# Kernel optimization log

Hardware: AMD Instinct MI355X
Metric: run time of the kernel (lower is better)

Reference implementation:

```python
import jax, jax.numpy as jnp
import numpy as np

N_NODES = 100000
N_EDGES = 3200000
EPS = 1e-5


def gcn_conv(x, edge_index, W, b):
    # PyG GCNConv: sym-normalized A+I, transform-then-propagate
    h = x @ W                                   # [N, out]
    src, dst = edge_index[0], edge_index[1]
    ones = jnp.ones(edge_index.shape[1], dtype=x.dtype)
    deg = jax.ops.segment_sum(ones, dst, num_segments=N_NODES) + 1.0  # +1 self-loop
    dis = jax.lax.rsqrt(deg)                    # deg^{-1/2}
    coef = (dis[src] * dis[dst])[:, None]
    agg = jax.ops.segment_sum(h[src] * coef, dst, num_segments=N_NODES)
    agg = agg + h * (dis * dis)[:, None]        # self-loop contribution
    return agg + b


def batch_norm(x, gamma, beta):
    mu = jnp.mean(x, axis=0)
    var = jnp.mean(jnp.square(x - mu), axis=0)
    return (x - mu) * jax.lax.rsqrt(var + EPS) * gamma + beta


def setup_inputs() -> dict:
    key = jax.random.key(0)
    ks = jax.random.split(key, 12)
    d = {
        "x": jax.random.normal(ks[0], (N_NODES, 256), dtype=jnp.float32),
        "edge_index": jax.random.randint(ks[1], (2, N_EDGES), 0, N_NODES, dtype=jnp.int32),
        "W1": jax.random.normal(ks[2], (256, 128), dtype=jnp.float32) * (1.0 / np.sqrt(256)),
        "b1": jnp.zeros((128,), jnp.float32),
        "g1": jnp.ones((128,), jnp.float32),
        "bt1": jnp.zeros((128,), jnp.float32),
        "W2": jax.random.normal(ks[3], (128, 64), dtype=jnp.float32) * (1.0 / np.sqrt(128)),
        "b2": jnp.zeros((64,), jnp.float32),
        "g2": jnp.ones((64,), jnp.float32),
        "bt2": jnp.zeros((64,), jnp.float32),
        "W3": jax.random.normal(ks[4], (64, 32), dtype=jnp.float32) * (1.0 / np.sqrt(64)),
        "b3": jnp.zeros((32,), jnp.float32),
        "g3": jnp.ones((32,), jnp.float32),
        "bt3": jnp.zeros((32,), jnp.float32),
        "Wfc": jax.random.normal(ks[5], (32, 1), dtype=jnp.float32) * (1.0 / np.sqrt(32)),
        "bfc": jnp.zeros((1,), jnp.float32),
    }
    return d


def reference(x, edge_index, W1, b1, g1, bt1, W2, b2, g2, bt2, W3, b3, g3, bt3, Wfc, bfc):
    h = jax.nn.relu(batch_norm(gcn_conv(x, edge_index, W1, b1), g1, bt1))
    h = jax.nn.relu(batch_norm(gcn_conv(h, edge_index, W2, b2), g2, bt2))
    h = jax.nn.relu(batch_norm(gcn_conv(h, edge_index, W3, b3), g3, bt3))
    return h @ Wfc + bfc
```

## Files before the change

kernel.cpp:

```cpp
#include <hip/hip_runtime.h>
#include <hip/hip_fp16.h>

#define EPS 1e-5f
constexpr int NT = 256;
constexpr int BSH = 9;
constexpr int BNODES = 1 << BSH;
constexpr int CH = 4096;

typedef _Float16 v8h __attribute__((ext_vector_type(8)));
typedef float v4f __attribute__((ext_vector_type(4)));


__global__ __launch_bounds__(NT) void bhist_kernel(const int* __restrict__ dst, int* __restrict__ gbhist,
                                                   int E, int NBUK) {
    __shared__ int h[512];
    int tid = threadIdx.x;
    for (int i = tid; i < 512; i += NT) h[i] = 0;
    __syncthreads();
    for (int e = blockIdx.x * NT + tid; e < E; e += gridDim.x * NT)
        atomicAdd(&h[dst[e] >> BSH], 1);
    __syncthreads();
    for (int i = tid; i < NBUK; i += NT)
        if (h[i]) atomicAdd(&gbhist[i], h[i]);
}


__global__ __launch_bounds__(NT) void bscan_kernel(const int* __restrict__ gbhist, int* __restrict__ bbase,
                                                   int* __restrict__ gcur, int E, int NBUK) {
    __shared__ int wsum[5];
    int tid = threadIdx.x;
    int lane = tid & 63, wid = tid >> 6;
    int e0 = (2 * tid < NBUK) ? gbhist[2 * tid] : 0;
    int e1 = (2 * tid + 1 < NBUK) ? gbhist[2 * tid + 1] : 0;
    int u = e0 + e1;
    int incl = u;
    #pragma unroll
    for (int off = 1; off < 64; off <<= 1) {
        int t = __shfl_up(incl, off, 64);
        if (lane >= off) incl += t;
    }
    if (lane == 63) wsum[wid] = incl;
    __syncthreads();
    if (tid == 0) { int s = 0; for (int w = 0; w < 4; w++) { int t = wsum[w]; wsum[w] = s; s += t; } }
    __syncthreads();
    int base = wsum[wid] + incl - u;
    if (2 * tid < NBUK)     { bbase[2 * tid] = base;          gcur[2 * tid] = base; }
    if (2 * tid + 1 < NBUK) { bbase[2 * tid + 1] = base + e0; gcur[2 * tid + 1] = base + e0; }
    if (tid == 0) bbase[NBUK] = E;
}


__global__ __launch_bounds__(NT) void part_kernel(const int* __restrict__ src, const int* __restrict__ dst,
                                                  int* __restrict__ gcur, int2* __restrict__ ebuf,
                                                  int E, int NBUK) {
    constexpr int EPT = CH / NT;
    __shared__ int hist[512];
    __shared__ int lscan[512];
    __shared__ int gbase[512];
    __shared__ int2 stage[CH];
    int tid = threadIdx.x;
    int lane = tid & 63;
    int e0 = blockIdx.x * CH;

    for (int i = tid; i < 512; i += NT) hist[i] = 0;
    __syncthreads();

    int2 ed[EPT]; int rank[EPT]; int buk[EPT];
    #pragma unroll
    for (int j = 0; j < EPT; j++) {
        int e = e0 + j * NT + tid;
        if (e < E) {
            ed[j].x = src[e]; ed[j].y = dst[e];
            buk[j] = ed[j].y >> BSH;
            rank[j] = atomicAdd(&hist[buk[j]], 1);
        } else buk[j] = -1;
    }
    __syncthreads();
    if (tid < 64) {
        int bi = tid * 8;
        int v[8]; int s = 0;
        #pragma unroll
        for (int j = 0; j < 8; j++) { v[j] = s; s += hist[bi + j]; }
        int incl = s;
        #pragma unroll
        for (int off = 1; off < 64; off <<= 1) {
            int t = __shfl_up(incl, off, 64);
            if (lane >= off) incl += t;
        }
        int lb = incl - s;
        #pragma unroll
        for (int j = 0; j < 8; j++) lscan[bi + j] = lb + v[j];
    }
    __syncthreads();
    for (int i = tid; i < NBUK; i += NT) {
        int c = hist[i];
        gbase[i] = c ? atomicAdd(&gcur[i], c) : 0;
    }
    #pragma unroll
    for (int j = 0; j < EPT; j++)
        if (buk[j] >= 0) stage[lscan[buk[j]] + rank[j]] = ed[j];
    __syncthreads();
    int cnt = min(E - e0, CH);
    for (int i = tid; i < cnt; i += NT) {
        int2 e = stage[i];
        int b = e.y >> BSH;
        ebuf[gbase[b] + (i - lscan[b])] = e;
    }
}


__global__ __launch_bounds__(NT) void bfill_kernel(const int2* __restrict__ ebuf, const int* __restrict__ bbase,
                                                   int* __restrict__ deg, int* __restrict__ row_start,
                                                   float* __restrict__ dis, int* __restrict__ csr, int N) {
    __shared__ int ldeg[BNODES];
    __shared__ int lrs[BNODES];
    __shared__ int wsum[5];
    int tid = threadIdx.x;
    int lane = tid & 63, wid = tid >> 6;
    int b = blockIdx.x;
    int node0 = b << BSH;
    int nn = min(BNODES, N - node0);
    int beg = bbase[b], end = bbase[b + 1];

    for (int i = tid; i < BNODES; i += NT) ldeg[i] = 0;
    __syncthreads();
    for (int i = beg + tid; i < end; i += NT)
        atomicAdd(&ldeg[ebuf[i].y - node0], 1);
    __syncthreads();
    int e0 = ldeg[2 * tid], e1 = ldeg[2 * tid + 1];
    int u = e0 + e1;
    int incl = u;
    #pragma unroll
    for (int off = 1; off < 64; off <<= 1) {
        int t = __shfl_up(incl, off, 64);
        if (lane >= off) incl += t;
    }
    if (lane == 63) wsum[wid] = incl;
    __syncthreads();
    if (tid == 0) { int s = 0; for (int w = 0; w < 4; w++) { int t = wsum[w]; wsum[w] = s; s += t; } }
    __syncthreads();
    int base = wsum[wid] + incl - u;
    lrs[2 * tid] = base;
    lrs[2 * tid + 1] = base + e0;
    __syncthreads();
    for (int i = tid; i < nn; i += NT) {
        int dg = ldeg[i];
        deg[node0 + i] = dg;
        row_start[node0 + i] = beg + lrs[i];
        dis[node0 + i] = rsqrtf((float)dg + 1.0f);
    }
    __syncthreads();
    for (int i = tid; i < BNODES; i += NT) ldeg[i] = 0;
    __syncthreads();
    for (int i = beg + tid; i < end; i += NT) {
        int2 e = ebuf[i];
        int l = e.y - node0;
        int off = atomicAdd(&ldeg[l], 1);
        csr[beg + lrs[l] + off] = e.x;
    }
}


__global__ __launch_bounds__(NT) void prepw_kernel(const float* __restrict__ W1, const float* __restrict__ W2,
                                                   const float* __restrict__ W3, __half* __restrict__ Wt1,
                                                   __half* __restrict__ Wt2, __half* __restrict__ Wt3) {
    int i = blockIdx.x * NT + threadIdx.x;
    if (i < 256 * 128) {
        int k = i >> 7, f = i & 127;
        Wt1[f * 256 + k] = __float2half(W1[i]);
    } else if (i < 256 * 128 + 128 * 64) {
        int j = i - 256 * 128; int k = j >> 6, f = j & 63;
        Wt2[f * 128 + k] = __float2half(W2[j]);
    } else if (i < 256 * 128 + 128 * 64 + 64 * 32) {
        int j = i - 256 * 128 - 128 * 64; int k = j >> 5, f = j & 31;
        Wt3[f * 64 + k] = __float2half(W3[j]);
    }
}


template<int K, int F, bool NORM>
__global__ __launch_bounds__(NT) void mgemm_kernel(const void* __restrict__ Xv, const __half* __restrict__ Wt,
                                                   const float* __restrict__ dis, const float* __restrict__ an,
                                                   const float* __restrict__ cn, __half* __restrict__ out, int N) {
    constexpr int KC = 32;
    constexpr int CG = F / 16;
    constexpr int LDA = KC + 8;
    constexpr int ASZ = NORM ? K : 1;
    __shared__ __half As[64 * LDA];
    __shared__ __half Bs[F * LDA];
    __shared__ float as_[ASZ], cs_[ASZ];

    int tid = threadIdx.x;
    if constexpr (NORM) {
        for (int i = tid; i < K; i += NT) { as_[i] = an[i]; cs_[i] = cn[i]; }
        __syncthreads();
    }
    int row0 = blockIdx.x * 64;
    int wid = tid >> 6, lane = tid & 63;
    int quad = lane >> 4, l16 = lane & 15;
    int tr = tid >> 3;
    int tk = (tid & 7) * 4;

    v4f acc[CG];
    #pragma unroll
    for (int g = 0; g < CG; g++) acc[g] = (v4f)0.f;

    for (int k0 = 0; k0 < K; k0 += KC) {
        #pragma unroll
        for (int r = tr; r < 64; r += 32) {
            int row = row0 + r;
            __half h0, h1, h2, h3;
            if (row < N) {
                if constexpr (NORM) {
                    const __half2* xp = (const __half2*)((const __half*)Xv + (size_t)row * K + k0 + tk);
                    float2 v0 = __half22float2(xp[0]);
                    float2 v1 = __half22float2(xp[1]);
                    h0 = __float2half(fmaxf(v0.x * as_[k0 + tk]     + cs_[k0 + tk],     0.f));
                    h1 = __float2half(fmaxf(v0.y * as_[k0 + tk + 1] + cs_[k0 + tk + 1], 0.f));
                    h2 = __float2half(fmaxf(v1.x * as_[k0 + tk + 2] + cs_[k0 + tk + 2], 0.f));
                    h3 = __float2half(fmaxf(v1.y * as_[k0 + tk + 3] + cs_[k0 + tk + 3], 0.f));
                } else {
                    float4 v = *(const float4*)((const float*)Xv + (size_t)row * K + k0 + tk);
                    h0 = __float2half(v.x); h1 = __float2half(v.y);
                    h2 = __float2half(v.z); h3 = __float2half(v.w);
                }
            } else {
                h0 = h1 = h2 = h3 = __float2half(0.f);
            }
            __half2* dst = (__half2*)&As[r * LDA + tk];
            dst[0] = __halves2half2(h0, h1);
            dst[1] = __halves2half2(h2, h3);
        }
        #pragma unroll
        for (int n = tr; n < F; n += 32) {
            const __half2* wp = (const __half2*)(Wt + (size_t)n * K + k0 + tk);
            __half2* dst = (__half2*)&Bs[n * LDA + tk];
            dst[0] = wp[0];
            dst[1] = wp[1];
        }
        __syncthreads();
        v8h a = *(const v8h*)&As[(wid * 16 + l16) * LDA + quad * 8];
        #pragma unroll
        for (int g = 0; g < CG; g++) {
            v8h b = *(const v8h*)&Bs[(g * 16 + l16) * LDA + quad * 8];
            acc[g] = __builtin_amdgcn_mfma_f32_16x16x32_f16(a, b, acc[g], 0, 0, 0);
        }
        __syncthreads();
    }
    #pragma unroll
    for (int reg = 0; reg < 4; reg++) {
        int row = row0 + wid * 16 + quad * 4 + reg;
        if (row < N) {
            float d = dis[row];
            #pragma unroll
            for (int g = 0; g < CG; g++)
                out[(size_t)row * F + g * 16 + l16] = __float2half(d * acc[g][reg]);
        }
    }
}


template<int F, int U>
__global__ __launch_bounds__(NT) void agg_kernel(const __half* __restrict__ hd, const int* __restrict__ csr,
                                                 const int* __restrict__ row_start, const int* __restrict__ deg,
                                                 const float* __restrict__ dis, const float* __restrict__ b,
                                                 __half* __restrict__ pre, int N) {
    constexpr int H = F / 2;
    constexpr int EPI = 64 / H;
    int wid = (blockIdx.x * NT + threadIdx.x) >> 6;
    int lane = threadIdx.x & 63;
    int fpos = lane % H;
    int sub = lane / H;
    if (wid >= N) return;
    int node = wid;
    int beg = row_start[node];
    int cnt = deg[node];
    const __half2* __restrict__ hd2 = (const __half2*)hd;

    float sx[U], sy[U];
    #pragma unroll
    for (int u = 0; u < U; u++) { sx[u] = 0.f; sy[u] = 0.f; }
    if (sub == 0) {
        float2 f = __half22float2(hd2[(size_t)node * H + fpos]);
        sx[0] = f.x; sy[0] = f.y;
    }
    int i = 0;
    for (; i + EPI * U <= cnt; i += EPI * U) {
        int srcs[U];
        #pragma unroll
        for (int u = 0; u < U; u++) srcs[u] = csr[beg + i + u * EPI + sub];
        #pragma unroll
        for (int u = 0; u < U; u++) {
            float2 f = __half22float2(hd2[(size_t)srcs[u] * H + fpos]);
            sx[u] += f.x; sy[u] += f.y;
        }
    }
    for (; i + sub < cnt; i += EPI) {
        int s = csr[beg + i + sub];
        float2 f = __half22float2(hd2[(size_t)s * H + fpos]);
        sx[0] += f.x; sy[0] += f.y;
    }
    #pragma unroll
    for (int u = 1; u < U; u++) { sx[0] += sx[u]; sy[0] += sy[u]; }
    #pragma unroll
    for (int m = H; m < 64; m <<= 1) {
        sx[0] += __shfl_xor(sx[0], m, 64);
        sy[0] += __shfl_xor(sy[0], m, 64);
    }
    if (sub == 0) {
        float d = dis[node];
        float2 bv = ((const float2*)b)[fpos];
        ((__half2*)pre)[(size_t)node * H + fpos] =
            __floats2half2_rn(d * sx[0] + bv.x, d * sy[0] + bv.y);
    }
}


template<int F>
__global__ __launch_bounds__(NT) void stats_kernel(const __half* __restrict__ pre, float* __restrict__ S1,
                                                   float* __restrict__ S2, int N) {
    constexpr int RPB = NT / F;
    int tid = threadIdx.x;
    int f = tid % F, r0 = tid / F;
    float s1 = 0.f, s2 = 0.f;
    for (int node = blockIdx.x * RPB + r0; node < N; node += gridDim.x * RPB) {
        float v = __half2float(pre[(size_t)node * F + f]);
        s1 += v; s2 += v * v;
    }
    __shared__ float l1[NT], l2[NT];
    l1[tid] = s1; l2[tid] = s2;
    __syncthreads();
    if (tid < F) {
        #pragma unroll
        for (int j = 1; j < RPB; j++) { s1 += l1[tid + j * F]; s2 += l2[tid + j * F]; }
        atomicAdd(&S1[tid], s1);
        atomicAdd(&S2[tid], s2);
    }
}

__global__ void params_kernel(const float* __restrict__ S1, const float* __restrict__ S2,
                              const float* __restrict__ g, const float* __restrict__ bt,
                              float* __restrict__ a, float* __restrict__ c, int N, int F) {
    int f = threadIdx.x;
    if (f < F) {
        float inv = 1.0f / (float)N;
        float mu = S1[f] * inv;
        float var = fmaxf(S2[f] * inv - mu * mu, 0.f);
        float av = g[f] * rsqrtf(var + EPS);
        a[f] = av;
        c[f] = bt[f] - mu * av;
    }
}


__global__ __launch_bounds__(NT) void fc_kernel(const __half* __restrict__ pre, const float* __restrict__ a,
                                                const float* __restrict__ c, const float* __restrict__ wfc,
                                                const float* __restrict__ bfc, float* __restrict__ out, int N) {
    __shared__ float wa[32], wc[32], ww[32];
    int tid = threadIdx.x;
    if (tid < 32) { wa[tid] = a[tid]; wc[tid] = c[tid]; ww[tid] = wfc[tid]; }
    __syncthreads();
    int n = blockIdx.x * NT + tid;
    if (n >= N) return;
    const __half2* p = (const __half2*)(pre + (size_t)n * 32);
    float acc = bfc[0];
    #pragma unroll
    for (int i = 0; i < 16; i++) {
        float2 v = __half22float2(p[i]);
        int f = i * 2;
        acc += fmaxf(v.x * wa[f] + wc[f], 0.f) * ww[f];
        acc += fmaxf(v.y * wa[f + 1] + wc[f + 1], 0.f) * ww[f + 1];
    }
    out[n] = acc;
}


extern "C" void kernel_launch(void* const* d_in, const int* in_sizes, int n_in,
                              void* d_out, int out_size, void* d_ws, size_t ws_size,
                              hipStream_t stream) {
    const float* x   = (const float*)d_in[0];
    const int*   ei  = (const int*)d_in[1];
    const float* W1  = (const float*)d_in[2];
    const float* b1  = (const float*)d_in[3];
    const float* g1  = (const float*)d_in[4];
    const float* bt1 = (const float*)d_in[5];
    const float* W2  = (const float*)d_in[6];
    const float* b2  = (const float*)d_in[7];
    const float* g2  = (const float*)d_in[8];
    const float* bt2 = (const float*)d_in[9];
    const float* W3  = (const float*)d_in[10];
    const float* b3  = (const float*)d_in[11];
    const float* g3  = (const float*)d_in[12];
    const float* bt3 = (const float*)d_in[13];
    const float* Wfc = (const float*)d_in[14];
    const float* bfc = (const float*)d_in[15];
    float* out = (float*)d_out;

    int N = in_sizes[0] / 256;
    int E = in_sizes[1] / 2;
    const int* src = ei;
    const int* dst = ei + E;
    int NBUK = (N + BNODES - 1) >> BSH;

    char* ws = (char*)d_ws;
    size_t off = 0;
    auto alloc = [&](size_t bytes) -> char* {
        char* p = ws + off;
        off += (bytes + 255) & ~(size_t)255;
        return p;
    };
    __half* bufA     = (__half*)alloc((size_t)N * 128 * 2);
    __half* bufB     = (__half*)alloc((size_t)N * 128 * 2);
    int2*  ebuf      = (int2*)alloc((size_t)E * 8);
    int*   csr       = (int*)alloc((size_t)E * 4);
    int*   deg       = (int*)alloc((size_t)N * 4);
    int*   row_start = (int*)alloc((size_t)N * 4);
    float* dis       = (float*)alloc((size_t)N * 4);
    int*   gbhist    = (int*)alloc((size_t)NBUK * 4);
    int*   bbase     = (int*)alloc((size_t)(NBUK + 1) * 4);
    int*   gcur      = (int*)alloc((size_t)NBUK * 4);
    __half* Wt1      = (__half*)alloc(256 * 128 * 2);
    __half* Wt2      = (__half*)alloc(128 * 64 * 2);
    __half* Wt3      = (__half*)alloc(64 * 32 * 2);
    float* stats = (float*)alloc(448 * 4 * 2);
    float* S1_1 = stats;       float* S2_1 = S1_1 + 128;
    float* S1_2 = S2_1 + 128;  float* S2_2 = S1_2 + 64;
    float* S1_3 = S2_2 + 64;   float* S2_3 = S1_3 + 32;
    float* a1 = S2_3 + 32; float* c1 = a1 + 128;
    float* a2 = c1 + 128;  float* c2 = a2 + 64;
    float* a3 = c2 + 64;   float* c3 = a3 + 32;

    hipMemsetAsync(gbhist, 0, (size_t)NBUK * 4, stream);
    hipMemsetAsync(stats, 0, 448 * 4, stream);

    bhist_kernel<<<512, NT, 0, stream>>>(dst, gbhist, E, NBUK);
    bscan_kernel<<<1, NT, 0, stream>>>(gbhist, bbase, gcur, E, NBUK);
    part_kernel<<<(E + CH - 1) / CH, NT, 0, stream>>>(src, dst, gcur, ebuf, E, NBUK);
    bfill_kernel<<<NBUK, NT, 0, stream>>>(ebuf, bbase, deg, row_start, dis, csr, N);
    prepw_kernel<<<(256 * 128 + 128 * 64 + 64 * 32 + NT - 1) / NT, NT, 0, stream>>>(W1, W2, W3, Wt1, Wt2, Wt3);

    int GB = (N + 63) / 64;
    int AB = (N + 3) / 4;
    int NB = (N + NT - 1) / NT;
    mgemm_kernel<256, 128, false><<<GB, NT, 0, stream>>>(x, Wt1, dis, nullptr, nullptr, bufA, N);
    agg_kernel<128, 4><<<AB, NT, 0, stream>>>(bufA, csr, row_start, deg, dis, b1, bufB, N);
    stats_kernel<128><<<256, NT, 0, stream>>>(bufB, S1_1, S2_1, N);
    params_kernel<<<1, 128, 0, stream>>>(S1_1, S2_1, g1, bt1, a1, c1, N, 128);
    mgemm_kernel<128, 64, true><<<GB, NT, 0, stream>>>(bufB, Wt2, dis, a1, c1, bufA, N);
    agg_kernel<64, 4><<<AB, NT, 0, stream>>>(bufA, csr, row_start, deg, dis, b2, bufB, N);
    stats_kernel<64><<<256, NT, 0, stream>>>(bufB, S1_2, S2_2, N);
    params_kernel<<<1, 64, 0, stream>>>(S1_2, S2_2, g2, bt2, a2, c2, N, 64);
    mgemm_kernel<64, 32, true><<<GB, NT, 0, stream>>>(bufB, Wt3, dis, a2, c2, bufA, N);
    agg_kernel<32, 2><<<AB, NT, 0, stream>>>(bufA, csr, row_start, deg, dis, b3, bufB, N);
    stats_kernel<32><<<256, NT, 0, stream>>>(bufB, S1_3, S2_3, N);
    params_kernel<<<1, 32, 0, stream>>>(S1_3, S2_3, g3, bt3, a3, c3, N, 32);
    fc_kernel<<<NB, NT, 0, stream>>>(bufB, a3, c3, Wfc, bfc, out, N);
}
```

Baseline: 683.5 us.

## Widen aggregation gathers to 16-byte loads and pack edge buffer into ints

The aggregation kernel now has each lane gather eight half-precision features with one 128-bit load, so one wavefront processes several edges at once. It still reduces across sub-groups with shuffles, and unroll factors are retuned per layer. The edge partition buffer packs the local destination offset and the source index into a single 32-bit word, halving its traffic, and the stats kernel reads half2 pairs. The packing assumes source indices fit in 18 bits and uses more registers per lane.

```diff
diff --git a/kernel.cpp b/kernel.cpp
--- a/kernel.cpp
+++ b/kernel.cpp
@@ -51,7 +51,7 @@
 
 
 __global__ __launch_bounds__(NT) void part_kernel(const int* __restrict__ src, const int* __restrict__ dst,
-                                                  int* __restrict__ gcur, int2* __restrict__ ebuf,
+                                                  int* __restrict__ gcur, int* __restrict__ ebuf,
                                                   int E, int NBUK) {
     constexpr int EPT = CH / NT;
     __shared__ int hist[512];
@@ -104,12 +104,12 @@
     for (int i = tid; i < cnt; i += NT) {
         int2 e = stage[i];
         int b = e.y >> BSH;
-        ebuf[gbase[b] + (i - lscan[b])] = e;
-    }
-}
-
-
-__global__ __launch_bounds__(NT) void bfill_kernel(const int2* __restrict__ ebuf, const int* __restrict__ bbase,
+        ebuf[gbase[b] + (i - lscan[b])] = ((e.y & (BNODES - 1)) << 18) | e.x;
+    }
+}
+
+
+__global__ __launch_bounds__(NT) void bfill_kernel(const int* __restrict__ ebuf, const int* __restrict__ bbase,
                                                    int* __restrict__ deg, int* __restrict__ row_start,
                                                    float* __restrict__ dis, int* __restrict__ csr, int N) {
     __shared__ int ldeg[BNODES];
@@ -125,7 +125,7 @@
     for (int i = tid; i < BNODES; i += NT) ldeg[i] = 0;
     __syncthreads();
     for (int i = beg + tid; i < end; i += NT)
-        atomicAdd(&ldeg[ebuf[i].y - node0], 1);
+        atomicAdd(&ldeg[ebuf[i] >> 18], 1);
     __syncthreads();
     int e0 = ldeg[2 * tid], e1 = ldeg[2 * tid + 1];
     int u = e0 + e1;
@@ -153,10 +153,10 @@
     for (int i = tid; i < BNODES; i += NT) ldeg[i] = 0;
     __syncthreads();
     for (int i = beg + tid; i < end; i += NT) {
-        int2 e = ebuf[i];
-        int l = e.y - node0;
+        int code = ebuf[i];
+        int l = code >> 18;
         int off = atomicAdd(&ldeg[l], 1);
-        csr[beg + lrs[l] + off] = e.x;
+        csr[beg + lrs[l] + off] = code & 0x3FFFF;
     }
 }
 
@@ -260,58 +260,72 @@
 }
 
 
+__device__ __forceinline__ void addh2(float* a, int4 v) {
+    float2 f0 = __half22float2(*(__half2*)&v.x);
+    float2 f1 = __half22float2(*(__half2*)&v.y);
+    float2 f2 = __half22float2(*(__half2*)&v.z);
+    float2 f3 = __half22float2(*(__half2*)&v.w);
+    a[0] += f0.x; a[1] += f0.y; a[2] += f1.x; a[3] += f1.y;
+    a[4] += f2.x; a[5] += f2.y; a[6] += f3.x; a[7] += f3.y;
+}
+
 template<int F, int U>
 __global__ __launch_bounds__(NT) void agg_kernel(const __half* __restrict__ hd, const int* __restrict__ csr,
                                                  const int* __restrict__ row_start, const int* __restrict__ deg,
                                                  const float* __restrict__ dis, const float* __restrict__ b,
                                                  __half* __restrict__ pre, int N) {
-    constexpr int H = F / 2;
-    constexpr int EPI = 64 / H;
-    int wid = (blockIdx.x * NT + threadIdx.x) >> 6;
+    constexpr int LR = F / 8;
+    constexpr int SUBS = 64 / LR;
+    int node = (blockIdx.x * NT + threadIdx.x) >> 6;
     int lane = threadIdx.x & 63;
-    int fpos = lane % H;
-    int sub = lane / H;
-    if (wid >= N) return;
-    int node = wid;
-    int beg = row_start[node];
-    int cnt = deg[node];
-    const __half2* __restrict__ hd2 = (const __half2*)hd;
-
-    float sx[U], sy[U];
-    #pragma unroll
-    for (int u = 0; u < U; u++) { sx[u] = 0.f; sy[u] = 0.f; }
+    int fl = lane % LR, sub = lane / LR;
+    if (node >= N) return;
+    int beg = row_start[node], cnt = deg[node];
+
+    float acc[U][8];
+    #pragma unroll
+    for (int u = 0; u < U; u++)
+        #pragma unroll
+        for (int j = 0; j < 8; j++) acc[u][j] = 0.f;
+
+    int i = 0;
+    for (; i + SUBS * U <= cnt; i += SUBS * U) {
+        int s[U];
+        #pragma unroll
+        for (int u = 0; u < U; u++) s[u] = csr[beg + i + u * SUBS + sub];
+        #pragma unroll
+        for (int u = 0; u < U; u++) {
+            int4 v = *(const int4*)(hd + (size_t)s[u] * F + fl * 8);
+            addh2(acc[u], v);
+        }
+    }
+    for (; i + sub < cnt; i += SUBS) {
+        int s = csr[beg + i + sub];
+        int4 v = *(const int4*)(hd + (size_t)s * F + fl * 8);
+        addh2(acc[0], v);
+    }
     if (sub == 0) {
-        float2 f = __half22float2(hd2[(size_t)node * H + fpos]);
-        sx[0] = f.x; sy[0] = f.y;
-    }
-    int i = 0;
-    for (; i + EPI * U <= cnt; i += EPI * U) {
-        int srcs[U];
-        #pragma unroll
-        for (int u = 0; u < U; u++) srcs[u] = csr[beg + i + u * EPI + sub];
-        #pragma unroll
-        for (int u = 0; u < U; u++) {
-            float2 f = __half22float2(hd2[(size_t)srcs[u] * H + fpos]);
-            sx[u] += f.x; sy[u] += f.y;
-        }
-    }
-    for (; i + sub < cnt; i += EPI) {
-        int s = csr[beg + i + sub];
-        float2 f = __half22float2(hd2[(size_t)s * H + fpos]);
-        sx[0] += f.x; sy[0] += f.y;
-    }
-    #pragma unroll
-    for (int u = 1; u < U; u++) { sx[0] += sx[u]; sy[0] += sy[u]; }
-    #pragma unroll
-    for (int m = H; m < 64; m <<= 1) {
-        sx[0] += __shfl_xor(sx[0], m, 64);
-        sy[0] += __shfl_xor(sy[0], m, 64);
-    }
+        int4 v = *(const int4*)(hd + (size_t)node * F + fl * 8);
+        addh2(acc[0], v);
+    }
+    #pragma unroll
+    for (int u = 1; u < U; u++)
+        #pragma unroll
+        for (int j = 0; j < 8; j++) acc[0][j] += acc[u][j];
+    #pragma unroll
+    for (int m = LR; m < 64; m <<= 1)
+        #pragma unroll
+        for (int j = 0; j < 8; j++) acc[0][j] += __shfl_xor(acc[0][j], m, 64);
     if (sub == 0) {
         float d = dis[node];
-        float2 bv = ((const float2*)b)[fpos];
-        ((__half2*)pre)[(size_t)node * H + fpos] =
-            __floats2half2_rn(d * sx[0] + bv.x, d * sy[0] + bv.y);
+        float4 b0 = *(const float4*)(b + fl * 8);
+        float4 b1 = *(const float4*)(b + fl * 8 + 4);
+        __half2 h[4];
+        h[0] = __floats2half2_rn(d * acc[0][0] + b0.x, d * acc[0][1] + b0.y);
+        h[1] = __floats2half2_rn(d * acc[0][2] + b0.z, d * acc[0][3] + b0.w);
+        h[2] = __floats2half2_rn(d * acc[0][4] + b1.x, d * acc[0][5] + b1.y);
+        h[3] = __floats2half2_rn(d * acc[0][6] + b1.z, d * acc[0][7] + b1.w);
+        *(int4*)(pre + (size_t)node * F + fl * 8) = *(int4*)h;
     }
 }
 
@@ -319,22 +333,27 @@
 template<int F>
 __global__ __launch_bounds__(NT) void stats_kernel(const __half* __restrict__ pre, float* __restrict__ S1,
                                                    float* __restrict__ S2, int N) {
-    constexpr int RPB = NT / F;
-    int tid = threadIdx.x;
-    int f = tid % F, r0 = tid / F;
-    float s1 = 0.f, s2 = 0.f;
+    constexpr int FP = F / 2;
+    constexpr int RPB = NT / FP;
+    int tid = threadIdx.x;
+    int f = tid % FP, r0 = tid / FP;
+    float s1x = 0.f, s1y = 0.f, s2x = 0.f, s2y = 0.f;
+    const __half2* p2 = (const __half2*)pre;
     for (int node = blockIdx.x * RPB + r0; node < N; node += gridDim.x * RPB) {
-        float v = __half2float(pre[(size_t)node * F + f]);
-        s1 += v; s2 += v * v;
-    }
-    __shared__ float l1[NT], l2[NT];
-    l1[tid] = s1; l2[tid] = s2;
-    __syncthreads();
-    if (tid < F) {
-        #pragma unroll
-        for (int j = 1; j < RPB; j++) { s1 += l1[tid + j * F]; s2 += l2[tid + j * F]; }
-        atomicAdd(&S1[tid], s1);
-        atomicAdd(&S2[tid], s2);
+        float2 v = __half22float2(p2[(size_t)node * FP + f]);
+        s1x += v.x; s1y += v.y; s2x += v.x * v.x; s2y += v.y * v.y;
+    }
+    __shared__ float l1x[NT], l1y[NT], l2x[NT], l2y[NT];
+    l1x[tid] = s1x; l1y[tid] = s1y; l2x[tid] = s2x; l2y[tid] = s2y;
+    __syncthreads();
+    if (tid < FP) {
+        #pragma unroll
+        for (int j = 1; j < RPB; j++) {
+            s1x += l1x[tid + j * FP]; s1y += l1y[tid + j * FP];
+            s2x += l2x[tid + j * FP]; s2y += l2y[tid + j * FP];
+        }
+        atomicAdd(&S1[2 * tid], s1x); atomicAdd(&S1[2 * tid + 1], s1y);
+        atomicAdd(&S2[2 * tid], s2x); atomicAdd(&S2[2 * tid + 1], s2y);
     }
 }
 
@@ -411,7 +430,7 @@
     };
     __half* bufA     = (__half*)alloc((size_t)N * 128 * 2);
     __half* bufB     = (__half*)alloc((size_t)N * 128 * 2);
-    int2*  ebuf      = (int2*)alloc((size_t)E * 8);
+    int*   ebuf      = (int*)alloc((size_t)E * 4);
     int*   csr       = (int*)alloc((size_t)E * 4);
     int*   deg       = (int*)alloc((size_t)N * 4);
     int*   row_start = (int*)alloc((size_t)N * 4);
@@ -447,11 +466,11 @@
     stats_kernel<128><<<256, NT, 0, stream>>>(bufB, S1_1, S2_1, N);
     params_kernel<<<1, 128, 0, stream>>>(S1_1, S2_1, g1, bt1, a1, c1, N, 128);
     mgemm_kernel<128, 64, true><<<GB, NT, 0, stream>>>(bufB, Wt2, dis, a1, c1, bufA, N);
-    agg_kernel<64, 4><<<AB, NT, 0, stream>>>(bufA, csr, row_start, deg, dis, b2, bufB, N);
+    agg_kernel<64, 2><<<AB, NT, 0, stream>>>(bufA, csr, row_start, deg, dis, b2, bufB, N);
     stats_kernel<64><<<256, NT, 0, stream>>>(bufB, S1_2, S2_2, N);
     params_kernel<<<1, 64, 0, stream>>>(S1_2, S2_2, g2, bt2, a2, c2, N, 64);
     mgemm_kernel<64, 32, true><<<GB, NT, 0, stream>>>(bufB, Wt3, dis, a2, c2, bufA, N);
-    agg_kernel<32, 2><<<AB, NT, 0, stream>>>(bufA, csr, row_start, deg, dis, b3, bufB, N);
+    agg_kernel<32, 1><<<AB, NT, 0, stream>>>(bufA, csr, row_start, deg, dis, b3, bufB, N);
     stats_kernel<32><<<256, NT, 0, stream>>>(bufB, S1_3, S2_3, N);
     params_kernel<<<1, 32, 0, stream>>>(S1_3, S2_3, g3, bt3, a3, c3, N, 32);
     fc_kernel<<<NB, NT, 0, stream>>>(bufB, a3, c3, Wfc, bfc, out, N);
```

Result: faster. 631.1 us (-7.7%).
